# Performance work log

Measured on AMD Instinct MI355X. Metric: run time of the kernel, lower is better.

Reference implementation:

```python
import jax, jax.numpy as jnp
import numpy as np


def setup_inputs() -> dict:
    key = jax.random.key(0)
    ks = jax.random.split(key, 8)
    N, C, T, V = 32, 64, 256, 25
    OUT, INTER, S = 64, 16, 3
    W_SCALE = 0.05  # keep complex softmax exp() well-conditioned
    return {
        "x_real": jax.random.normal(ks[0], (N, C, T, V), jnp.float32),
        "x_imag": jax.random.normal(ks[1], (N, C, T, V), jnp.float32),
        "A": jax.random.uniform(ks[2], (S, V, V), jnp.float32),
        "PA": jax.random.normal(ks[3], (S, V, V), jnp.float32) * 1e-3,
        "Wa": jax.random.normal(ks[4], (S, 2 * INTER, 2 * C), jnp.float32) * W_SCALE,
        "ba": jnp.zeros((S, 2 * INTER), jnp.float32),
        "Wb": jax.random.normal(ks[5], (S, 2 * INTER, 2 * C), jnp.float32) * W_SCALE,
        "bb": jnp.zeros((S, 2 * INTER), jnp.float32),
        "Wd": jax.random.normal(ks[6], (S, 2 * OUT, 2 * C), jnp.float32) * W_SCALE,
        "bd": jnp.zeros((S, 2 * OUT), jnp.float32),
        "bn_weight": jnp.ones((OUT,), jnp.float32),
        "bn_bias": jnp.zeros((OUT,), jnp.float32),
    }


def _cconv1x1(z, W, b):
    # C_Conv2d with k=1: 1x1 conv over concat(real, imag) channels.
    zc = jnp.concatenate([z.real, z.imag], axis=1)          # [N, 2*Cin, T, V]
    o = jnp.einsum("oc,nctv->notv", W, zc) + b[None, :, None, None]
    h = W.shape[0] // 2
    return jax.lax.complex(o[:, :h], o[:, h:])              # [N, Cout, T, V] complex


def _forward(x_real, x_imag, A, PA, Wa, ba, Wb, bb, Wd, bd, bn_weight, bn_bias):
    x = jax.lax.complex(x_real, x_imag)                     # [N, C, T, V]
    N, C, T, V = x.shape
    inter = Wa.shape[1] // 2
    Afull = A + PA                                          # [3, V, V] real
    X2 = x.reshape(N, C * T, V)
    y = None
    for i in range(A.shape[0]):
        A1 = _cconv1x1(x, Wa[i], ba[i])                     # [N, inter, T, V]
        A1 = A1.transpose(0, 3, 1, 2).reshape(N, V, inter * T)
        A2 = _cconv1x1(x, Wb[i], bb[i]).reshape(N, inter * T, V)
        S = jnp.matmul(A1, A2) / (inter * T)                # [N, V, V] complex
        # complex softmax over dim=1 (no max-subtraction, faithful to C_softmax)
        ez = jnp.exp(S)
        S = ez / jnp.sum(ez, axis=1, keepdims=True)
        S = S + Afull[i]
        z = jnp.matmul(X2, S).reshape(N, C, T, V)
        z = _cconv1x1(z, Wd[i], bd[i])                      # [N, OUT, T, V]
        y = z if y is None else y + z
    # C_BatchNorm2d on complex input: complex mean, real variance = E|y-mu|^2
    mu = jnp.mean(y, axis=(0, 2, 3))                        # [OUT] complex
    var = jnp.mean(jnp.abs(y - mu[None, :, None, None]) ** 2, axis=(0, 2, 3))
    yn = (y - mu[None, :, None, None]) / jnp.sqrt(var + 1e-5)[None, :, None, None]
    yn = yn * bn_weight[None, :, None, None] + bn_bias[None, :, None, None]
    yn = yn + x  # down = identity (in_channels == out_channels)
    return jnp.stack([yn.real, yn.imag])                    # [2, N, OUT, T, V] real


def reference(x_real, x_imag, A, PA, Wa, ba, Wb, bb, Wd, bd, bn_weight, bn_bias):
    return _forward(x_real, x_imag, A, PA, Wa, ba, Wb, bb, Wd, bd, bn_weight, bn_bias)
```

## Files before the change

kernel.cpp:

```cpp
#include <hip/hip_runtime.h>
#include <hip/hip_bf16.h>
#include <stdint.h>

#define NN 32
#define CC 64
#define TTOT 256
#define VV 25
#define NS 3
constexpr int TV  = TTOT * VV;
constexpr int CTV = CC * TV;
constexpr size_t PLANE = (size_t)NN * CTV;

typedef unsigned short ushort_t;
using short8 = __attribute__((ext_vector_type(8))) short;
using f32x4  = __attribute__((ext_vector_type(4))) float;

static __device__ __forceinline__ ushort_t f2bf(float f) {
  __hip_bfloat16 h = __float2bfloat16(f);
  return reinterpret_cast<ushort_t&>(h);
}
static __device__ __forceinline__ float bf2f(ushort_t h) {
  union { uint32_t u; float f; } v; v.u = ((uint32_t)h) << 16;
  return v.f;
}
static __device__ __forceinline__ int SWZ(int row, int k) {
  return ((row << 7) + k) ^ ((row & 7) << 3);
}
static __device__ __forceinline__ f32x4 mfma16(short8 a, short8 b, f32x4 c) {
  return __builtin_amdgcn_mfma_f32_16x16x32_bf16(a, b, c, 0, 0, 0);
}
static __device__ __forceinline__ short8 negbf8(short8 x) {
  short8 r;
#pragma unroll
  for (int j = 0; j < 8; ++j) r[j] = x[j] ^ (short)0x8000;
  return r;
}

__global__ __launch_bounds__(256) void k0_wfrag(
    const float* __restrict__ Wd, const float* __restrict__ Wa,
    const float* __restrict__ Wb, ushort_t* __restrict__ wfrag,
    ushort_t* __restrict__ wab)
{
  const int i = blockIdx.x;
  for (int e = threadIdx.x; e < 16384; e += 256) {
    int ot = e >> 11, m = (e >> 9) & 3, l = (e >> 3) & 63, j = e & 7;
    int r  = ot * 16 + (l & 15);
    int c = m * 16 + ((l >> 4) << 2) + (j >> 1), comp = j & 1;
    wfrag[(size_t)i * 16384 + e] = f2bf(Wd[(size_t)i * 16384 + r * 128 + comp * 64 + c]);
  }
  for (int e = threadIdx.x; e < 8192; e += 256) {
    int mt = e >> 11, ks = (e >> 9) & 3, l = (e >> 3) & 63, j = e & 7;
    int r  = mt * 16 + (l & 15);
    int kp = ks * 32 + ((l >> 4) << 3) + j;
    float v = (r < 32) ? Wa[((size_t)i * 32 + r) * 128 + kp]
                       : Wb[((size_t)i * 32 + (r - 32)) * 128 + kp];
    wab[(size_t)i * 8192 + e] = f2bf(v);
  }
}

__global__ __launch_bounds__(256) void k1_spart(
    const float* __restrict__ xr, const float* __restrict__ xi,
    const ushort_t* __restrict__ wab, const float* __restrict__ ba,
    const float* __restrict__ bb, float* __restrict__ Spart)
{
  const int tc = blockIdx.x, n = blockIdx.y;
  const int tid = threadIdx.x, lane = tid & 63, wv = tid >> 6;
  const int r16 = lane & 15, gw = lane >> 4;
  __shared__ alignas(16) ushort_t zc[128 * 128];
  __shared__ alignas(16) ushort_t Ga[32 * 128];
  __shared__ alignas(16) ushort_t Gb[32 * 128];

  for (int e4 = tid; e4 < 128 * 25; e4 += 256) {
    int c = e4 / 25, q = e4 % 25;
    const float* src = (c < 64) ? xr : xi;
    float4 w = *(const float4*)&src[(size_t)n * CTV + (c & 63) * TV + tc * 100 + q * 4];
#pragma unroll
    for (int jj = 0; jj < 4; ++jj) {
      int g = q * 4 + jj, t = g / 25, v = g - t * 25;
      zc[SWZ(t * 32 + v, c)] = f2bf(((const float*)&w)[jj]);
    }
  }
  for (int e = tid; e < 28 * 128; e += 256) {
    int r7 = e >> 7, c = e & 127;
    int t = r7 / 7, vv = 25 + r7 % 7;
    zc[SWZ(t * 32 + vv, c)] = 0;
  }

  const int mu = wv >> 1, nv = wv & 1;

  for (int i = 0; i < NS; ++i) {
    __syncthreads();

    {
      short8 afr[4];
#pragma unroll
      for (int ks = 0; ks < 4; ++ks)
        afr[ks] = *(const short8*)&wab[((((size_t)i * 4 + wv) * 4 + ks) * 64 + lane) * 8];
      float bias[4];
#pragma unroll
      for (int j = 0; j < 4; ++j) {
        int row = wv * 16 + gw * 4 + j;
        bias[j] = (row < 32) ? ba[i * 32 + row] : bb[i * 32 + (row - 32)];
      }
      ushort_t* gbuf = (wv < 2) ? Ga : Gb;
      const int half = (wv & 1) * 64;
      for (int nt = 0; nt < 8; ++nt) {
        f32x4 acc = {0.f, 0.f, 0.f, 0.f};
        const int brow = nt * 16 + r16;
#pragma unroll
        for (int ks = 0; ks < 4; ++ks) {
          short8 bfr = *(const short8*)&zc[SWZ(brow, ks * 32 + gw * 8)];
          acc = mfma16(afr[ks], bfr, acc);
        }
        int pos2 = nt * 16 + r16;
        int t = pos2 >> 5, v = pos2 & 31;
        int k0w = half + t * 16 + gw * 4;
        uint32_t w0 = (uint32_t)f2bf(acc[0] + bias[0]) | ((uint32_t)f2bf(acc[1] + bias[1]) << 16);
        uint32_t w1 = (uint32_t)f2bf(acc[2] + bias[2]) | ((uint32_t)f2bf(acc[3] + bias[3]) << 16);
        uint2 pk; pk.x = w0; pk.y = w1;
        *(uint2*)&gbuf[SWZ(v, k0w)] = pk;
      }
    }
    __syncthreads();

    {
      const int urow = mu * 16 + r16;
      const int vrow = nv * 16 + r16;
      f32x4 Prr = {0.f,0.f,0.f,0.f}, Pii = {0.f,0.f,0.f,0.f};
      f32x4 Pri = {0.f,0.f,0.f,0.f}, Pir = {0.f,0.f,0.f,0.f};
#pragma unroll
      for (int ks = 0; ks < 2; ++ks) {
        int ko = ks * 32 + gw * 8;
        short8 arF = *(const short8*)&Ga[SWZ(urow, ko)];
        short8 aiF = *(const short8*)&Ga[SWZ(urow, 64 + ko)];
        short8 brF = *(const short8*)&Gb[SWZ(vrow, ko)];
        short8 biF = *(const short8*)&Gb[SWZ(vrow, 64 + ko)];
        Prr = mfma16(arF, brF, Prr);
        Pii = mfma16(aiF, biF, Pii);
        Pri = mfma16(arF, biF, Pri);
        Pir = mfma16(aiF, brF, Pir);
      }
#pragma unroll
      for (int j = 0; j < 4; ++j) {
        int u = mu * 16 + gw * 4 + j;
        int v = nv * 16 + r16;
        if (u < VV && v < VV) {
          size_t idx = ((((size_t)i * NN + n) * 64 + tc) * 625 + u * 25 + v) * 2;
          Spart[idx]     = Prr[j] - Pii[j];
          Spart[idx + 1] = Pri[j] + Pir[j];
        }
      }
    }
  }
}

__global__ __launch_bounds__(256) void k2_softmax(
    const float* __restrict__ Spart, const float* __restrict__ Aw,
    const float* __restrict__ PA, ushort_t* __restrict__ sfrag)
{
  const int i = blockIdx.x, n = blockIdx.y, tid = threadIdx.x;
  __shared__ float ez[625 * 2];
  __shared__ float den[25 * 2];
  for (int e = tid; e < 625; e += 256) {
    float sr = 0.f, si = 0.f;
    const float* p = Spart + (((size_t)i * NN + n) * 64 * 625 + e) * 2;
    for (int tcb = 0; tcb < 64; ++tcb) { sr += p[0]; si += p[1]; p += 625 * 2; }
    sr *= (1.f / 4096.f); si *= (1.f / 4096.f);
    float m = expf(sr);
    ez[e * 2] = m * cosf(si);
    ez[e * 2 + 1] = m * sinf(si);
  }
  __syncthreads();
  if (tid < 25) {
    float dr = 0.f, di = 0.f;
    for (int u = 0; u < 25; ++u) { dr += ez[(u * 25 + tid) * 2]; di += ez[(u * 25 + tid) * 2 + 1]; }
    float inv = 1.f / (dr * dr + di * di);
    den[tid * 2] = dr * inv; den[tid * 2 + 1] = -di * inv;
  }
  __syncthreads();
  for (int e = tid; e < 625; e += 256) {
    int v = e % 25;
    float er = ez[e * 2], ei = ez[e * 2 + 1];
    float dr = den[v * 2], di = den[v * 2 + 1];
    float outr = er * dr - ei * di + Aw[i * 625 + e] + PA[i * 625 + e];
    float outi = er * di + ei * dr;
    ez[e * 2] = outr; ez[e * 2 + 1] = outi;
  }
  __syncthreads();
  for (int e = tid; e < 512; e += 256) {
    int l = e & 63, nt = (e >> 6) & 1, m = e >> 7;
    int u0 = (l >> 4) << 3, v = nt * 16 + (l & 15);
    short8 pk;
#pragma unroll
    for (int j = 0; j < 8; ++j) {
      int u = u0 + j;
      float val = 0.f;
      if (u < VV && v < VV) {
        float sr_ = ez[(u * 25 + v) * 2], si_ = ez[(u * 25 + v) * 2 + 1];
        float base = (m < 2) ? sr_ : si_;
        if (m & 1) { float hi = bf2f(f2bf(base)); val = base - hi; }
        else val = base;
      }
      pk[j] = (short)f2bf(val);
    }
    *(short8*)&sfrag[((size_t)(i * NN + n) * 512 + e) * 8] = pk;
  }
}

__global__ __launch_bounds__(512, 2) void k3_y(
    const float* __restrict__ xr, const float* __restrict__ xi,
    const ushort_t* __restrict__ sfrag, const ushort_t* __restrict__ wfrag,
    const float* __restrict__ bd, float* __restrict__ out,
    float* __restrict__ bnpart)
{
  const int tq = blockIdx.x, n = blockIdx.y;
  const int tid = threadIdx.x, lane = tid & 63, wv = tid >> 6;
  const int r16 = lane & 15, gw = lane >> 4;
  __shared__ alignas(16) ushort_t wlds[49152];
  __shared__ float stats[8][128][2];

  {
    ushort_t* xs = wlds;
    for (int e4 = tid; e4 < 128 * 50; e4 += 512) {
      int c = e4 / 50, q = e4 % 50;
      const float* src = (c < 64) ? xr : xi;
      float4 w = *(const float4*)&src[(size_t)n * CTV + (c & 63) * TV + tq * 200 + q * 4];
#pragma unroll
      for (int jj = 0; jj < 4; ++jj) {
        int g = q * 4 + jj, t = g / 25, u = g - t * 25;
        xs[(t >> 2) * 16384 + SWZ(c, (t & 3) * 32 + u)] = f2bf(((const float*)&w)[jj]);
      }
    }
    for (int e = tid; e < 128 * 56; e += 512) {
      int c = e / 56, r = e % 56;
      int t = r / 7, u = 25 + r % 7;
      xs[(t >> 2) * 16384 + SWZ(c, (t & 3) * 32 + u)] = 0;
    }
  }
  __syncthreads();

  const int tl = wv & 3, th = wv >> 2;
  const int kx = tl * 32 + gw * 8;
  short8 axr[4], axi[4];
#pragma unroll
  for (int tile = 0; tile < 4; ++tile) {
    axr[tile] = *(const short8*)&wlds[th * 16384 + SWZ(tile * 16 + r16, kx)];
    axi[tile] = *(const short8*)&wlds[th * 16384 + SWZ(64 + tile * 16 + r16, kx)];
  }
  __syncthreads();

  {
    short8 tmp[12];
#pragma unroll
    for (int q = 0; q < 12; ++q)
      tmp[q] = *(const short8*)&wfrag[(size_t)(q * 512 + tid) * 8];
#pragma unroll
    for (int q = 0; q < 12; ++q)
      *(short8*)&wlds[(size_t)(q * 512 + tid) * 8] = tmp[q];
  }
  __syncthreads();

  f32x4 acc[8][2];
#pragma unroll
  for (int a = 0; a < 8; ++a) { acc[a][0] = {0.f,0.f,0.f,0.f}; acc[a][1] = {0.f,0.f,0.f,0.f}; }

  auto load_sf = [&](int i, short8 sf[4][2]) {
    const ushort_t* sb = sfrag + (size_t)(i * NN + n) * 4096;
#pragma unroll
    for (int m = 0; m < 4; ++m)
#pragma unroll
      for (int nt = 0; nt < 2; ++nt)
        sf[m][nt] = *(const short8*)&sb[((m * 2 + nt) * 64 + lane) * 8];
  };
  auto compute_i = [&](int i, short8 sf[4][2]) {
    short8 sn0[2], sn1[2];
#pragma unroll
    for (int nt = 0; nt < 2; ++nt) { sn0[nt] = negbf8(sf[2][nt]); sn1[nt] = negbf8(sf[3][nt]); }
    short8 bp[4][2];
#pragma unroll
    for (int tile = 0; tile < 4; ++tile) {
#pragma unroll
      for (int nt = 0; nt < 2; ++nt) {
        f32x4 zr = {0.f,0.f,0.f,0.f}, zi = {0.f,0.f,0.f,0.f};
        zr = mfma16(axr[tile], sf[0][nt], zr);
        zr = mfma16(axr[tile], sf[1][nt], zr);
        zr = mfma16(axi[tile], sn0[nt], zr);
        zr = mfma16(axi[tile], sn1[nt], zr);
        zi = mfma16(axr[tile], sf[2][nt], zi);
        zi = mfma16(axr[tile], sf[3][nt], zi);
        zi = mfma16(axi[tile], sf[0][nt], zi);
        zi = mfma16(axi[tile], sf[1][nt], zi);
        short8 pk;
#pragma unroll
        for (int j = 0; j < 4; ++j) {
          pk[2 * j]     = (short)f2bf(zr[j]);
          pk[2 * j + 1] = (short)f2bf(zi[j]);
        }
        bp[tile][nt] = pk;
      }
    }
#pragma unroll
    for (int ot = 0; ot < 8; ++ot) {
#pragma unroll
      for (int m = 0; m < 4; ++m) {
        short8 a = *(const short8*)&wlds[((size_t)i * 16384) + (size_t)((ot * 4 + m) * 64 + lane) * 8];
        acc[ot][0] = mfma16(a, bp[m][0], acc[ot][0]);
        acc[ot][1] = mfma16(a, bp[m][1], acc[ot][1]);
      }
    }
  };

  short8 sfA[4][2], sfB[4][2];
  load_sf(0, sfA);
  load_sf(1, sfB);
  compute_i(0, sfA);
  load_sf(2, sfA);
  compute_i(1, sfB);
  compute_i(2, sfA);

  const int t = tq * 8 + wv;
#pragma unroll
  for (int ot = 0; ot < 8; ++ot) {
#pragma unroll
    for (int j = 0; j < 4; ++j) {
      int row = ot * 16 + gw * 4 + j;
      float bias = bd[row] + bd[128 + row] + bd[256 + row];
      float s = 0.f, q = 0.f;
#pragma unroll
      for (int nt = 0; nt < 2; ++nt) {
        int v = nt * 16 + r16;
        float val = acc[ot][nt][j] + bias;
        if (v < VV) {
          out[(size_t)(row >> 6) * PLANE + (size_t)n * CTV + (row & 63) * TV + t * VV + v] = val;
          s += val; q += val * val;
        }
      }
#pragma unroll
      for (int d = 1; d < 16; d <<= 1) { s += __shfl_xor(s, d); q += __shfl_xor(q, d); }
      if (r16 == 0) { stats[wv][row][0] = s; stats[wv][row][1] = q; }
    }
  }
  __syncthreads();
  if (tid < 128) {
    float s = 0.f, q = 0.f;
#pragma unroll
    for (int w = 0; w < 8; ++w) { s += stats[w][tid][0]; q += stats[w][tid][1]; }
    size_t b = (size_t)n * 32 + tq;
    bnpart[(b * 128 + tid) * 2]     = s;
    bnpart[(b * 128 + tid) * 2 + 1] = q;
  }
}

__global__ __launch_bounds__(256) void k4_stats(
    const float* __restrict__ bnpart, const float* __restrict__ bnw,
    const float* __restrict__ bnb, float* __restrict__ coeff)
{
  const int o = blockIdx.x, tid = threadIdx.x;
  float sr = 0.f, qr = 0.f, si = 0.f, qi = 0.f;
  for (int b = tid; b < 1024; b += 256) {
    const float* p = bnpart + ((size_t)b * 128 + o) * 2;
    sr += p[0]; qr += p[1];
    const float* p2 = bnpart + ((size_t)b * 128 + 64 + o) * 2;
    si += p2[0]; qi += p2[1];
  }
#pragma unroll
  for (int d = 1; d < 64; d <<= 1) {
    sr += __shfl_xor(sr, d); qr += __shfl_xor(qr, d);
    si += __shfl_xor(si, d); qi += __shfl_xor(qi, d);
  }
  __shared__ float red[4][4];
  int lane = tid & 63, wv = tid >> 6;
  if (lane == 0) { red[wv][0] = sr; red[wv][1] = qr; red[wv][2] = si; red[wv][3] = qi; }
  __syncthreads();
  if (tid == 0) {
    sr = red[0][0] + red[1][0] + red[2][0] + red[3][0];
    qr = red[0][1] + red[1][1] + red[2][1] + red[3][1];
    si = red[0][2] + red[1][2] + red[2][2] + red[3][2];
    qi = red[0][3] + red[1][3] + red[2][3] + red[3][3];
    const float invM = 1.f / (float)((size_t)NN * TTOT * VV);
    float mur = sr * invM, mui = si * invM;
    float var = (qr + qi) * invM - mur * mur - mui * mui;
    float inv = rsqrtf(var + 1e-5f);
    coeff[o * 4 + 0] = mur; coeff[o * 4 + 1] = mui;
    coeff[o * 4 + 2] = inv * bnw[o]; coeff[o * 4 + 3] = bnb[o];
  }
}

__global__ __launch_bounds__(256) void k5_norm(
    const float* __restrict__ xr, const float* __restrict__ xi,
    const float* __restrict__ coeff, float* __restrict__ out)
{
  size_t idx0 = ((size_t)blockIdx.x * 256 + threadIdx.x) * 4;
  size_t stride = (size_t)gridDim.x * 256 * 4;
  for (size_t e = idx0; e < PLANE; e += stride) {
    int o = (int)((e / TV) & 63);
    float4 cf = *(const float4*)&coeff[o * 4];
    float4 yr = *(float4*)&out[e];
    float4 yi = *(float4*)&out[PLANE + e];
    float4 vr = *(const float4*)&xr[e];
    float4 vi = *(const float4*)&xi[e];
    yr.x = (yr.x - cf.x) * cf.z + cf.w + vr.x;
    yr.y = (yr.y - cf.x) * cf.z + cf.w + vr.y;
    yr.z = (yr.z - cf.x) * cf.z + cf.w + vr.z;
    yr.w = (yr.w - cf.x) * cf.z + cf.w + vr.w;
    yi.x = (yi.x - cf.y) * cf.z + vi.x;
    yi.y = (yi.y - cf.y) * cf.z + vi.y;
    yi.z = (yi.z - cf.y) * cf.z + vi.z;
    yi.w = (yi.w - cf.y) * cf.z + vi.w;
    *(float4*)&out[e] = yr;
    *(float4*)&out[PLANE + e] = yi;
  }
}

extern "C" void kernel_launch(void* const* d_in, const int* in_sizes, int n_in,
                              void* d_out, int out_size, void* d_ws, size_t ws_size,
                              hipStream_t stream) {
  const float* xr  = (const float*)d_in[0];
  const float* xi  = (const float*)d_in[1];
  const float* Aw  = (const float*)d_in[2];
  const float* PA  = (const float*)d_in[3];
  const float* Wa  = (const float*)d_in[4];
  const float* ba  = (const float*)d_in[5];
  const float* Wb  = (const float*)d_in[6];
  const float* bb  = (const float*)d_in[7];
  const float* Wd  = (const float*)d_in[8];
  const float* bd  = (const float*)d_in[9];
  const float* bnw = (const float*)d_in[10];
  const float* bnb = (const float*)d_in[11];
  float* out = (float*)d_out;
  float* ws = (float*)d_ws;

  float*    Spart  = ws;
  float*    bnpart = ws;
  ushort_t* sfrag  = (ushort_t*)(ws + 7680000);
  ushort_t* wfrag  = (ushort_t*)(ws + 7876608);
  ushort_t* wab    = (ushort_t*)(ws + 7901184);
  float*    coeff  = ws + 7913472;

  k0_wfrag<<<NS, 256, 0, stream>>>(Wd, Wa, Wb, wfrag, wab);
  k1_spart<<<dim3(64, NN), 256, 0, stream>>>(xr, xi, wab, ba, bb, Spart);
  k2_softmax<<<dim3(NS, NN), 256, 0, stream>>>(Spart, Aw, PA, sfrag);
  k3_y<<<dim3(32, NN), 512, 0, stream>>>(xr, xi, sfrag, wfrag, bd, out, bnpart);
  k4_stats<<<64, 256, 0, stream>>>(bnpart, bnw, bnb, coeff);
  k5_norm<<<6400, 256, 0, stream>>>(xr, xi, coeff, out);
}
```

Measured before the change: 245.2 us.

## Drop split-bf16 softmax residual and double-buffer Wd weights in LDS for occupancy

The softmax matrix is no longer stored as a bf16 hi/lo pair. Only a single bf16 real and imaginary fragment is kept, which halves the first-stage MFMAs and the sfrag traffic. The y kernel's LDS weight buffer shrinks from three full Wd slices to two, streamed in a double-buffered pattern, and launch bounds are raised to allow 4 blocks per CU. The intent is lower LDS use and higher occupancy. The cost is extra barriers and reduced precision in the mixing matrix, which may affect accuracy.

```diff
diff --git a/kernel.cpp b/kernel.cpp
--- a/kernel.cpp
+++ b/kernel.cpp
@@ -187,7 +187,7 @@
     ez[e * 2] = outr; ez[e * 2 + 1] = outi;
   }
   __syncthreads();
-  for (int e = tid; e < 512; e += 256) {
+  for (int e = tid; e < 256; e += 256) {
     int l = e & 63, nt = (e >> 6) & 1, m = e >> 7;
     int u0 = (l >> 4) << 3, v = nt * 16 + (l & 15);
     short8 pk;
@@ -195,19 +195,15 @@
     for (int j = 0; j < 8; ++j) {
       int u = u0 + j;
       float val = 0.f;
-      if (u < VV && v < VV) {
-        float sr_ = ez[(u * 25 + v) * 2], si_ = ez[(u * 25 + v) * 2 + 1];
-        float base = (m < 2) ? sr_ : si_;
-        if (m & 1) { float hi = bf2f(f2bf(base)); val = base - hi; }
-        else val = base;
-      }
+      if (u < VV && v < VV)
+        val = (m == 0) ? ez[(u * 25 + v) * 2] : ez[(u * 25 + v) * 2 + 1];
       pk[j] = (short)f2bf(val);
     }
-    *(short8*)&sfrag[((size_t)(i * NN + n) * 512 + e) * 8] = pk;
-  }
-}
-
-__global__ __launch_bounds__(512, 2) void k3_y(
+    *(short8*)&sfrag[((size_t)(i * NN + n) * 256 + e) * 8] = pk;
+  }
+}
+
+__global__ __launch_bounds__(512, 4) void k3_y(
     const float* __restrict__ xr, const float* __restrict__ xi,
     const ushort_t* __restrict__ sfrag, const ushort_t* __restrict__ wfrag,
     const float* __restrict__ bd, float* __restrict__ out,
@@ -216,11 +212,11 @@
   const int tq = blockIdx.x, n = blockIdx.y;
   const int tid = threadIdx.x, lane = tid & 63, wv = tid >> 6;
   const int r16 = lane & 15, gw = lane >> 4;
-  __shared__ alignas(16) ushort_t wlds[49152];
+  __shared__ alignas(16) ushort_t wbuf[2][16384];
   __shared__ float stats[8][128][2];
 
   {
-    ushort_t* xs = wlds;
+    ushort_t* xs = &wbuf[0][0];
     for (int e4 = tid; e4 < 128 * 50; e4 += 512) {
       int c = e4 / 50, q = e4 % 50;
       const float* src = (c < 64) ? xr : xi;
@@ -244,19 +240,17 @@
   short8 axr[4], axi[4];
 #pragma unroll
   for (int tile = 0; tile < 4; ++tile) {
-    axr[tile] = *(const short8*)&wlds[th * 16384 + SWZ(tile * 16 + r16, kx)];
-    axi[tile] = *(const short8*)&wlds[th * 16384 + SWZ(64 + tile * 16 + r16, kx)];
+    axr[tile] = *(const short8*)&wbuf[th][SWZ(tile * 16 + r16, kx)];
+    axi[tile] = *(const short8*)&wbuf[th][SWZ(64 + tile * 16 + r16, kx)];
   }
   __syncthreads();
 
   {
-    short8 tmp[12];
-#pragma unroll
-    for (int q = 0; q < 12; ++q)
-      tmp[q] = *(const short8*)&wfrag[(size_t)(q * 512 + tid) * 8];
-#pragma unroll
-    for (int q = 0; q < 12; ++q)
-      *(short8*)&wlds[(size_t)(q * 512 + tid) * 8] = tmp[q];
+    short8 tmp[4];
+#pragma unroll
+    for (int q = 0; q < 4; ++q) tmp[q] = *(const short8*)&wfrag[(size_t)(q * 512 + tid) * 8];
+#pragma unroll
+    for (int q = 0; q < 4; ++q) *(short8*)&wbuf[0][(q * 512 + tid) * 8] = tmp[q];
   }
   __syncthreads();
 
@@ -264,32 +258,27 @@
 #pragma unroll
   for (int a = 0; a < 8; ++a) { acc[a][0] = {0.f,0.f,0.f,0.f}; acc[a][1] = {0.f,0.f,0.f,0.f}; }
 
-  auto load_sf = [&](int i, short8 sf[4][2]) {
-    const ushort_t* sb = sfrag + (size_t)(i * NN + n) * 4096;
-#pragma unroll
-    for (int m = 0; m < 4; ++m)
+  auto load_sf = [&](int i, short8 sf[2][2]) {
+    const ushort_t* sb = sfrag + (size_t)(i * NN + n) * 2048;
+#pragma unroll
+    for (int m = 0; m < 2; ++m)
 #pragma unroll
       for (int nt = 0; nt < 2; ++nt)
         sf[m][nt] = *(const short8*)&sb[((m * 2 + nt) * 64 + lane) * 8];
   };
-  auto compute_i = [&](int i, short8 sf[4][2]) {
-    short8 sn0[2], sn1[2];
-#pragma unroll
-    for (int nt = 0; nt < 2; ++nt) { sn0[nt] = negbf8(sf[2][nt]); sn1[nt] = negbf8(sf[3][nt]); }
-    short8 bp[4][2];
+  auto phaseA = [&](short8 sf[2][2], short8 bp[4][2]) {
+    short8 snI[2];
+#pragma unroll
+    for (int nt = 0; nt < 2; ++nt) snI[nt] = negbf8(sf[1][nt]);
 #pragma unroll
     for (int tile = 0; tile < 4; ++tile) {
 #pragma unroll
       for (int nt = 0; nt < 2; ++nt) {
         f32x4 zr = {0.f,0.f,0.f,0.f}, zi = {0.f,0.f,0.f,0.f};
         zr = mfma16(axr[tile], sf[0][nt], zr);
-        zr = mfma16(axr[tile], sf[1][nt], zr);
-        zr = mfma16(axi[tile], sn0[nt], zr);
-        zr = mfma16(axi[tile], sn1[nt], zr);
-        zi = mfma16(axr[tile], sf[2][nt], zi);
-        zi = mfma16(axr[tile], sf[3][nt], zi);
+        zr = mfma16(axi[tile], snI[nt], zr);
+        zi = mfma16(axr[tile], sf[1][nt], zi);
         zi = mfma16(axi[tile], sf[0][nt], zi);
-        zi = mfma16(axi[tile], sf[1][nt], zi);
         short8 pk;
 #pragma unroll
         for (int j = 0; j < 4; ++j) {
@@ -299,24 +288,42 @@
         bp[tile][nt] = pk;
       }
     }
+  };
+  auto phaseB = [&](const ushort_t* wlds, short8 bp[4][2]) {
 #pragma unroll
     for (int ot = 0; ot < 8; ++ot) {
 #pragma unroll
       for (int m = 0; m < 4; ++m) {
-        short8 a = *(const short8*)&wlds[((size_t)i * 16384) + (size_t)((ot * 4 + m) * 64 + lane) * 8];
+        short8 a = *(const short8*)&wlds[(size_t)((ot * 4 + m) * 64 + lane) * 8];
         acc[ot][0] = mfma16(a, bp[m][0], acc[ot][0]);
         acc[ot][1] = mfma16(a, bp[m][1], acc[ot][1]);
       }
     }
   };
 
-  short8 sfA[4][2], sfB[4][2];
-  load_sf(0, sfA);
-  load_sf(1, sfB);
-  compute_i(0, sfA);
-  load_sf(2, sfA);
-  compute_i(1, sfB);
-  compute_i(2, sfA);
+  short8 sf[2][2], bp[4][2], tmp[4];
+
+#pragma unroll
+  for (int q = 0; q < 4; ++q) tmp[q] = *(const short8*)&wfrag[16384 + (size_t)(q * 512 + tid) * 8];
+  load_sf(0, sf);
+  phaseA(sf, bp);
+#pragma unroll
+  for (int q = 0; q < 4; ++q) *(short8*)&wbuf[1][(q * 512 + tid) * 8] = tmp[q];
+  phaseB(&wbuf[0][0], bp);
+  __syncthreads();
+
+#pragma unroll
+  for (int q = 0; q < 4; ++q) tmp[q] = *(const short8*)&wfrag[32768 + (size_t)(q * 512 + tid) * 8];
+  load_sf(1, sf);
+  phaseA(sf, bp);
+#pragma unroll
+  for (int q = 0; q < 4; ++q) *(short8*)&wbuf[0][(q * 512 + tid) * 8] = tmp[q];
+  phaseB(&wbuf[1][0], bp);
+  __syncthreads();
+
+  load_sf(2, sf);
+  phaseA(sf, bp);
+  phaseB(&wbuf[0][0], bp);
 
   const int t = tq * 8 + wv;
 #pragma unroll
@@ -433,9 +440,9 @@
   float*    Spart  = ws;
   float*    bnpart = ws;
   ushort_t* sfrag  = (ushort_t*)(ws + 7680000);
-  ushort_t* wfrag  = (ushort_t*)(ws + 7876608);
-  ushort_t* wab    = (ushort_t*)(ws + 7901184);
-  float*    coeff  = ws + 7913472;
+  ushort_t* wfrag  = (ushort_t*)(ws + 7778304);
+  ushort_t* wab    = (ushort_t*)(ws + 7802880);
+  float*    coeff  = ws + 7815168;
 
   k0_wfrag<<<NS, 256, 0, stream>>>(Wd, Wa, Wb, wfrag, wab);
   k1_spart<<<dim3(64, NN), 256, 0, stream>>>(xr, xi, wab, ba, bb, Spart);
```

Measured after the change: 267.6 us. 1.09x slower.
